# Optimization experiments

Hardware: AMD Instinct MI355X
Metric: run time of the kernel (lower is better)

## Reference

```python
import jax, jax.numpy as jnp
import numpy as np


def _resize_bilinear_ac(x, Ht, Wt):
    # bilinear resize with align_corners=True; x: [B,C,h,w] -> [B,C,Ht,Wt]
    B, C, h, w = x.shape
    ys = jnp.linspace(0.0, h - 1.0, Ht)
    xs = jnp.linspace(0.0, w - 1.0, Wt)
    y0 = jnp.floor(ys).astype(jnp.int32)
    y1 = jnp.minimum(y0 + 1, h - 1)
    x0 = jnp.floor(xs).astype(jnp.int32)
    x1 = jnp.minimum(x0 + 1, w - 1)
    wy = (ys - y0).astype(x.dtype)[None, None, :, None]
    wx = (xs - x0).astype(x.dtype)[None, None, None, :]
    r0 = x[:, :, y0, :]
    r1 = x[:, :, y1, :]
    v00 = r0[:, :, :, x0]; v01 = r0[:, :, :, x1]
    v10 = r1[:, :, :, x0]; v11 = r1[:, :, :, x1]
    return (1 - wy) * ((1 - wx) * v00 + wx * v01) + wy * ((1 - wx) * v10 + wx * v11)


def _grid_sample_zeros_ac(img, grid):
    # F.grid_sample(mode='bilinear', padding_mode='zeros', align_corners=True)
    # img: [B,C,H,W], grid: [B,H,W,2] in [-1,1] (x, y)
    B, C, H, W = img.shape
    x = (grid[..., 0] + 1.0) * 0.5 * (W - 1)  # [B,H,W] pixel coords
    y = (grid[..., 1] + 1.0) * 0.5 * (H - 1)
    x0 = jnp.floor(x)
    y0 = jnp.floor(y)
    wx = (x - x0)[:, None]  # [B,1,H,W]
    wy = (y - y0)[:, None]

    def gather(xi, yi):
        valid = ((xi >= 0) & (xi <= W - 1) & (yi >= 0) & (yi <= H - 1)).astype(img.dtype)
        xc = jnp.clip(xi, 0, W - 1).astype(jnp.int32)
        yc = jnp.clip(yi, 0, H - 1).astype(jnp.int32)
        v = jax.vmap(lambda im, yy, xx: im[:, yy, xx])(img, yc, xc)  # [B,C,H,W]
        return v * valid[:, None]

    v00 = gather(x0, y0)
    v01 = gather(x0 + 1, y0)
    v10 = gather(x0, y0 + 1)
    v11 = gather(x0 + 1, y0 + 1)
    return (1 - wy) * ((1 - wx) * v00 + wx * v01) + wy * ((1 - wx) * v10 + wx * v11)


def setup_inputs() -> dict:
    key = jax.random.key(0)
    k1, k2, k3 = jax.random.split(key, 3)
    B, C, H, W = 8, 3, 384, 1280
    h, w = 96, 320
    image = jax.random.normal(k1, (B, C, H, W), dtype=jnp.float32)
    # positive disparity (fraction of width, scaled by W inside forward)
    disp = jax.random.uniform(k2, (B, 1, h, w), dtype=jnp.float32, minval=0.01, maxval=0.3)
    scene = jax.random.normal(k3, (B, 3, h, w), dtype=jnp.float32) * 0.1
    K = jnp.array([[371.0, 0.0, 320.0], [0.0, 371.0, 96.0], [0.0, 0.0, 1.0]], dtype=jnp.float32)
    intrinsic = jnp.tile(K[None], (B, 1, 1))
    aug_size = jnp.tile(jnp.array([192.0, 640.0], dtype=jnp.float32)[None], (B, 1))
    return {"image": image, "disp": disp, "scene": scene, "intrinsic": intrinsic, "aug_size": aug_size}


def reference(image, disp, scene, intrinsic, aug_size):
    B, C, H, W = image.shape
    # interpolate_as(disp, image) * W
    disp_full = _resize_bilinear_ac(disp, H, W) * W
    # rel_scale = local_scale / aug_size, local_scale = (H, W)
    rel = jnp.array([H, W], dtype=aug_size.dtype) / aug_size  # [B,2] = (sy, sx)
    sy, sx = rel[:, 0], rel[:, 1]
    fx = intrinsic[:, 0, 0] * sx
    fy = intrinsic[:, 1, 1] * sy
    cx = intrinsic[:, 0, 2] * sx
    cy = intrinsic[:, 1, 2] * sy
    z = jnp.zeros_like(fx)
    o = jnp.ones_like(fx)
    K = jnp.stack([jnp.stack([fx, z, cx], 1),
                   jnp.stack([z, fy, cy], 1),
                   jnp.stack([z, z, o], 1)], 1)  # [B,3,3]
    # disp2depth_stereo_clamp
    depth = jnp.clip(fx[:, None, None, None] * 0.54 / (disp_full + 1e-8), 0.001, 80.0)
    # pixel2point
    xg, yg = jnp.meshgrid(jnp.arange(W, dtype=jnp.float32), jnp.arange(H, dtype=jnp.float32))  # [H,W]
    pix = jnp.stack([xg.ravel(), yg.ravel(), jnp.ones(H * W, dtype=jnp.float32)], 0)  # [3,HW]
    Kinv = jnp.linalg.inv(K)
    point = jnp.einsum('bij,jn->bin', Kinv, pix) * depth.reshape(B, 1, -1)  # [B,3,HW]
    # point2pixel_ms
    scene_full = _resize_bilinear_ac(scene, H, W)
    point_form = point.reshape(B, 3, H, W) + scene_full
    proj = jnp.einsum('bij,bjn->bin', K, point_form.reshape(B, 3, -1))
    coord = (proj[:, 0:2] / (proj[:, 2:3] + 1e-8)).reshape(B, 2, H, W)
    nx = coord[:, 0] / (W - 1) * 2.0 - 1.0
    ny = coord[:, 1] / (H - 1) * 2.0 - 1.0
    grid = jnp.stack([nx, ny], -1)  # [B,H,W,2]
    return _grid_sample_zeros_ac(image, grid)
```

## Files before the change

kernel.cpp:

```cpp
#include <hip/hip_runtime.h>
#include <hip/hip_fp16.h>

#define BATCH 8
#define CH 3
#define H_OUT 384
#define W_OUT 1280
#define H_IN 96
#define W_IN 320
#define HW_OUT (H_OUT * W_OUT)
#define HW_IN (H_IN * W_IN)

#define ROWS_PT 2
#define SEGS_PER_ROW (W_OUT / 256)
#define PAIRS (H_OUT / ROWS_PT)
#define CHUNKS_PER_B (PAIRS * SEGS_PER_ROW)

#define LCOLS 68
#define LROWS 3

#define PSTRIDE 1282
#define PK_HALVES ((size_t)(1 + (size_t)BATCH * H_OUT * PSTRIDE) * 4)
#define PK_BYTES (PK_HALVES * 2)

struct __attribute__((packed, aligned(4))) f2 { float x, y; };
struct __attribute__((packed, aligned(8))) h8 { unsigned int w[4]; };

__global__ __launch_bounds__(256) void pack_kernel(
    const float* __restrict__ image, __half* __restrict__ pk)
{
    int i = blockIdx.x * 256 + threadIdx.x;
    int b = i / HW_OUT;
    int p = i - b * HW_OUT;
    int y = p / W_OUT;
    int x = p - y * W_OUT;
    const float* ib = image + (size_t)b * (CH * HW_OUT) + p;
    float c0 = ib[0];
    float c1 = ib[HW_OUT];
    float c2 = ib[2 * HW_OUT];
    __half2 lo = __floats2half2_rn(c0, c1);
    __half2 hi = __floats2half2_rn(c2, 0.0f);
    uint2 v;
    v.x = *reinterpret_cast<unsigned int*>(&lo);
    v.y = *reinterpret_cast<unsigned int*>(&hi);
    __half* pd = pk + 4;
    size_t row = (size_t)b * H_OUT + y;
    *reinterpret_cast<uint2*>(pd + (row * PSTRIDE + x) * 4) = v;

    if (i < BATCH * H_OUT) {
        uint2 z; z.x = 0u; z.y = 0u;
        size_t r = (size_t)i;
        *reinterpret_cast<uint2*>(pd + (r * PSTRIDE + 1280) * 4) = z;
        *reinterpret_cast<uint2*>(pd + (r * PSTRIDE + 1281) * 4) = z;
        if (i == 0) *reinterpret_cast<uint2*>(pk) = z;
    }
}

template <bool PACKED>
__global__ __launch_bounds__(256) void warp_sceneflow_kernel(
    const float* __restrict__ image,
    const __half* __restrict__ pk,
    const float* __restrict__ disp,
    const float* __restrict__ scene,
    const float* __restrict__ intrin,
    const float* __restrict__ aug,
    float* __restrict__ out)
{
    int bid = blockIdx.x;
    int b = bid & 7;
    int c = bid >> 3;
    int yp = c / SEGS_PER_ROW;
    int xseg = c - yp * SEGS_PER_ROW;
    int x = xseg * 256 + threadIdx.x;
    int ybase = yp * ROWS_PT;

    __shared__ float4 lds4[LROWS][LCOLS];
    int ylo = (int)((float)ybase * ((float)(H_IN - 1) / (float)(H_OUT - 1)));
    int xlo = (int)((float)(xseg * 256) * ((float)(W_IN - 1) / (float)(W_OUT - 1)));
    if (threadIdx.x < LROWS * LCOLS) {
        int row = threadIdx.x / LCOLS;
        int col = threadIdx.x - row * LCOLS;
        int gy = min(ylo + row, H_IN - 1);
        int gx = min(xlo + col, W_IN - 1);
        int gi = gy * W_IN + gx;
        const float* dp = disp + b * HW_IN;
        const float* sp = scene + b * (CH * HW_IN);
        float4 v;
        v.x = dp[gi];
        v.y = sp[gi];
        v.z = sp[HW_IN + gi];
        v.w = sp[2 * HW_IN + gi];
        lds4[row][col] = v;
    }
    __syncthreads();

    float sy = (float)H_OUT / aug[b * 2 + 0];
    float sxs = (float)W_OUT / aug[b * 2 + 1];
    float fx = intrin[b * 9 + 0] * sxs;
    float fy = intrin[b * 9 + 4] * sy;
    float cx = intrin[b * 9 + 2] * sxs;
    float cy = intrin[b * 9 + 5] * sy;
    float inv_fx = 1.0f / fx;
    float inv_fy = 1.0f / fy;

    float xsrc = (float)x * ((float)(W_IN - 1) / (float)(W_OUT - 1));
    int x0 = (int)xsrc;
    float wx = xsrc - (float)x0;
    int lx = x0 - xlo;

    float g00[ROWS_PT], g01[ROWS_PT], g10[ROWS_PT], g11[ROWS_PT];
    int rb0[ROWS_PT], rb1[ROWS_PT];
    bool rc[ROWS_PT], lc[ROWS_PT];

    #pragma unroll
    for (int r = 0; r < ROWS_PT; ++r) {
        int y = ybase + r;
        float ysrc = (float)y * ((float)(H_IN - 1) / (float)(H_OUT - 1));
        int y0 = (int)ysrc;
        float wy = ysrc - (float)y0;
        int ly = y0 - ylo;

        float4 t00 = lds4[ly][lx];
        float4 t01 = lds4[ly][lx + 1];
        float4 t10 = lds4[ly + 1][lx];
        float4 t11 = lds4[ly + 1][lx + 1];

        float w00 = (1.0f - wy) * (1.0f - wx);
        float w01 = (1.0f - wy) * wx;
        float w10 = wy * (1.0f - wx);
        float w11 = wy * wx;

        float dval = w00 * t00.x + w01 * t01.x + w10 * t10.x + w11 * t11.x;
        float sc0  = w00 * t00.y + w01 * t01.y + w10 * t10.y + w11 * t11.y;
        float sc1  = w00 * t00.z + w01 * t01.z + w10 * t10.z + w11 * t11.z;
        float sc2  = w00 * t00.w + w01 * t01.w + w10 * t10.w + w11 * t11.w;

        float disp_full = dval * (float)W_OUT;
        float depth = fminf(fmaxf(fx * 0.54f / (disp_full + 1e-8f), 0.001f), 80.0f);

        float X = ((float)x - cx) * inv_fx * depth + sc0;
        float Y = ((float)y - cy) * inv_fy * depth + sc1;
        float Z = depth + sc2;
        float u = fx * X + cx * Z;
        float v = fy * Y + cy * Z;
        float rw = 1.0f / (Z + 1e-8f);
        float gx = u * rw;
        float gy = v * rw;

        float gx0f = floorf(gx), gy0f = floorf(gy);
        float fwx = gx - gx0f, fwy = gy - gy0f;
        int ix0 = (int)gx0f, iy0 = (int)gy0f;
        int ix1 = ix0 + 1, iy1 = iy0 + 1;
        bool vx0 = (ix0 >= 0) && (ix0 <= W_OUT - 1);
        bool vx1 = (ix1 >= 0) && (ix1 <= W_OUT - 1);
        bool vy0 = (iy0 >= 0) && (iy0 <= H_OUT - 1);
        bool vy1 = (iy1 >= 0) && (iy1 <= H_OUT - 1);
        int cy0 = min(max(iy0, 0), H_OUT - 1);
        int cy1 = min(max(iy1, 0), H_OUT - 1);
        g00[r] = (1.0f - fwy) * (1.0f - fwx) * ((vx0 && vy0) ? 1.0f : 0.0f);
        g01[r] = (1.0f - fwy) * fwx * ((vx1 && vy0) ? 1.0f : 0.0f);
        g10[r] = fwy * (1.0f - fwx) * ((vx0 && vy1) ? 1.0f : 0.0f);
        g11[r] = fwy * fwx * ((vx1 && vy1) ? 1.0f : 0.0f);

        if constexpr (PACKED) {
            int bx = min(max(ix0, -1), W_OUT - 1);
            rb0[r] = ((b * H_OUT + cy0) * PSTRIDE + bx);
            rb1[r] = ((b * H_OUT + cy1) * PSTRIDE + bx);
        } else {
            int cx0 = min(max(ix0, 0), W_OUT - 1);
            int cx1 = min(max(ix1, 0), W_OUT - 1);
            int xbi = min(cx0, W_OUT - 2);
            rc[r] = (cx0 != xbi);
            lc[r] = (cx1 == xbi);
            rb0[r] = cy0 * W_OUT + xbi;
            rb1[r] = cy1 * W_OUT + xbi;
        }
    }

    float res[ROWS_PT][CH];
    if constexpr (PACKED) {
        const __half* pd = pk + 4;
        #pragma unroll
        for (int r = 0; r < ROWS_PT; ++r) {
            h8 L0 = *reinterpret_cast<const h8*>(pd + (size_t)rb0[r] * 4);
            h8 L1 = *reinterpret_cast<const h8*>(pd + (size_t)rb1[r] * 4);
            __half2 h0a = *reinterpret_cast<__half2*>(&L0.w[0]);
            __half2 h0b = *reinterpret_cast<__half2*>(&L0.w[1]);
            __half2 h1a = *reinterpret_cast<__half2*>(&L0.w[2]);
            __half2 h1b = *reinterpret_cast<__half2*>(&L0.w[3]);
            __half2 k0a = *reinterpret_cast<__half2*>(&L1.w[0]);
            __half2 k0b = *reinterpret_cast<__half2*>(&L1.w[1]);
            __half2 k1a = *reinterpret_cast<__half2*>(&L1.w[2]);
            __half2 k1b = *reinterpret_cast<__half2*>(&L1.w[3]);
            res[r][0] = g00[r] * __low2float(h0a) + g01[r] * __low2float(h1a)
                      + g10[r] * __low2float(k0a) + g11[r] * __low2float(k1a);
            res[r][1] = g00[r] * __high2float(h0a) + g01[r] * __high2float(h1a)
                      + g10[r] * __high2float(k0a) + g11[r] * __high2float(k1a);
            res[r][2] = g00[r] * __low2float(h0b) + g01[r] * __low2float(h1b)
                      + g10[r] * __low2float(k0b) + g11[r] * __low2float(k1b);
        }
    } else {
        const float* ib = image + (size_t)b * (CH * HW_OUT);
        const float* im0 = ib;
        const float* im1 = ib + HW_OUT;
        const float* im2 = ib + 2 * HW_OUT;
        #pragma unroll
        for (int r = 0; r < ROWS_PT; ++r) {
            f2 P0 = *(const f2*)(im0 + rb0[r]); f2 P1 = *(const f2*)(im0 + rb1[r]);
            f2 Q0 = *(const f2*)(im1 + rb0[r]); f2 Q1 = *(const f2*)(im1 + rb1[r]);
            f2 T0 = *(const f2*)(im2 + rb0[r]); f2 T1 = *(const f2*)(im2 + rb1[r]);
            float p00 = rc[r] ? P0.y : P0.x, p01 = lc[r] ? P0.x : P0.y;
            float p10 = rc[r] ? P1.y : P1.x, p11 = lc[r] ? P1.x : P1.y;
            float q00 = rc[r] ? Q0.y : Q0.x, q01 = lc[r] ? Q0.x : Q0.y;
            float q10 = rc[r] ? Q1.y : Q1.x, q11 = lc[r] ? Q1.x : Q1.y;
            float t00 = rc[r] ? T0.y : T0.x, t01 = lc[r] ? T0.x : T0.y;
            float t10 = rc[r] ? T1.y : T1.x, t11 = lc[r] ? T1.x : T1.y;
            res[r][0] = g00[r] * p00 + g01[r] * p01 + g10[r] * p10 + g11[r] * p11;
            res[r][1] = g00[r] * q00 + g01[r] * q01 + g10[r] * q10 + g11[r] * q11;
            res[r][2] = g00[r] * t00 + g01[r] * t01 + g10[r] * t10 + g11[r] * t11;
        }
    }

    float* ob = out + (size_t)b * (CH * HW_OUT);
    #pragma unroll
    for (int r = 0; r < ROWS_PT; ++r) {
        int op = (ybase + r) * W_OUT + x;
        __builtin_nontemporal_store(res[r][0], ob + op);
        __builtin_nontemporal_store(res[r][1], ob + HW_OUT + op);
        __builtin_nontemporal_store(res[r][2], ob + 2 * HW_OUT + op);
    }
}

extern "C" void kernel_launch(void* const* d_in, const int* in_sizes, int n_in,
                              void* d_out, int out_size, void* d_ws, size_t ws_size,
                              hipStream_t stream) {
    const float* image  = (const float*)d_in[0];
    const float* disp   = (const float*)d_in[1];
    const float* scene  = (const float*)d_in[2];
    const float* intrin = (const float*)d_in[3];
    const float* aug    = (const float*)d_in[4];
    float* out = (float*)d_out;

    const int grid = BATCH * CHUNKS_PER_B;

    if (ws_size >= PK_BYTES) {
        __half* pk = (__half*)d_ws;
        pack_kernel<<<BATCH * HW_OUT / 256, 256, 0, stream>>>(image, pk);
        warp_sceneflow_kernel<true><<<grid, 256, 0, stream>>>(
            image, pk, disp, scene, intrin, aug, out);
    } else {
        warp_sceneflow_kernel<false><<<grid, 256, 0, stream>>>(
            image, nullptr, disp, scene, intrin, aug, out);
    }
}
```

Baseline: 54.66 us.

## Pack vertically adjacent row pairs so each bilinear tap pair is one 16-byte load

Adds a row-pair packed layout in fp16 where each entry holds a pixel's three channels for rows y-1 and y, padded with a zero border. The gather then needs two aligned 16-byte loads per output instead of two loads spread across separate rows. Blending is done with half2 FMAs instead of fp32 math. In exchange the workspace is about twice as large and the pack kernel reads each image row twice, and fp16 accumulation adds precision error.

```diff
diff --git a/kernel.cpp b/kernel.cpp
--- a/kernel.cpp
+++ b/kernel.cpp
@@ -18,14 +18,60 @@
 #define LCOLS 68
 #define LROWS 3
 
-#define PSTRIDE 1282
-#define PK_HALVES ((size_t)(1 + (size_t)BATCH * H_OUT * PSTRIDE) * 4)
-#define PK_BYTES (PK_HALVES * 2)
+#define P1STRIDE 1282
+#define P1_HALVES ((size_t)(1 + (size_t)BATCH * H_OUT * P1STRIDE) * 4)
+#define P1_BYTES (P1_HALVES * 2)
+
+#define RP_STRIDE 1282
+#define RP_ROWS (H_OUT + 1)
+#define RP_EPB ((size_t)RP_ROWS * RP_STRIDE)
+#define RP_ENTRIES ((size_t)BATCH * RP_EPB)
+#define RP_BYTES (RP_ENTRIES * 16)
 
 struct __attribute__((packed, aligned(4))) f2 { float x, y; };
 struct __attribute__((packed, aligned(8))) h8 { unsigned int w[4]; };
-
-__global__ __launch_bounds__(256) void pack_kernel(
+struct __attribute__((aligned(16))) h16 { unsigned int w[4]; };
+
+static __device__ __forceinline__ __half2 u2h2(unsigned int u) {
+    return *reinterpret_cast<__half2*>(&u);
+}
+
+__global__ __launch_bounds__(256) void pack_rowpair_kernel(
+    const float* __restrict__ image, __half* __restrict__ pk)
+{
+    size_t i = (size_t)blockIdx.x * 256 + threadIdx.x;
+    if (i >= RP_ENTRIES) return;
+    int b = (int)(i / RP_EPB);
+    int rem = (int)(i - (size_t)b * RP_EPB);
+    int e = rem / RP_STRIDE;
+    int cxi = rem - e * RP_STRIDE;
+    int x = cxi - 1;
+
+    __half2 p0 = __floats2half2_rn(0.0f, 0.0f);
+    __half2 p1 = p0, p2 = p0, p3 = p0;
+    if (x >= 0 && x < W_OUT) {
+        const float* ib = image + (size_t)b * (CH * HW_OUT);
+        int y0 = e - 1, y1 = e;
+        if (y0 >= 0) {
+            int o = y0 * W_OUT + x;
+            p0 = __floats2half2_rn(ib[o], ib[HW_OUT + o]);
+            p1 = __floats2half2_rn(ib[2 * HW_OUT + o], 0.0f);
+        }
+        if (y1 < H_OUT) {
+            int o = y1 * W_OUT + x;
+            p2 = __floats2half2_rn(ib[o], ib[HW_OUT + o]);
+            p3 = __floats2half2_rn(ib[2 * HW_OUT + o], 0.0f);
+        }
+    }
+    h16 v;
+    v.w[0] = *reinterpret_cast<unsigned int*>(&p0);
+    v.w[1] = *reinterpret_cast<unsigned int*>(&p1);
+    v.w[2] = *reinterpret_cast<unsigned int*>(&p2);
+    v.w[3] = *reinterpret_cast<unsigned int*>(&p3);
+    *reinterpret_cast<h16*>(pk + i * 8) = v;
+}
+
+__global__ __launch_bounds__(256) void pack_single_kernel(
     const float* __restrict__ image, __half* __restrict__ pk)
 {
     int i = blockIdx.x * 256 + threadIdx.x;
@@ -34,28 +80,24 @@
     int y = p / W_OUT;
     int x = p - y * W_OUT;
     const float* ib = image + (size_t)b * (CH * HW_OUT) + p;
-    float c0 = ib[0];
-    float c1 = ib[HW_OUT];
-    float c2 = ib[2 * HW_OUT];
-    __half2 lo = __floats2half2_rn(c0, c1);
-    __half2 hi = __floats2half2_rn(c2, 0.0f);
+    __half2 lo = __floats2half2_rn(ib[0], ib[HW_OUT]);
+    __half2 hi = __floats2half2_rn(ib[2 * HW_OUT], 0.0f);
     uint2 v;
     v.x = *reinterpret_cast<unsigned int*>(&lo);
     v.y = *reinterpret_cast<unsigned int*>(&hi);
     __half* pd = pk + 4;
     size_t row = (size_t)b * H_OUT + y;
-    *reinterpret_cast<uint2*>(pd + (row * PSTRIDE + x) * 4) = v;
-
+    *reinterpret_cast<uint2*>(pd + (row * P1STRIDE + x) * 4) = v;
     if (i < BATCH * H_OUT) {
         uint2 z; z.x = 0u; z.y = 0u;
         size_t r = (size_t)i;
-        *reinterpret_cast<uint2*>(pd + (r * PSTRIDE + 1280) * 4) = z;
-        *reinterpret_cast<uint2*>(pd + (r * PSTRIDE + 1281) * 4) = z;
+        *reinterpret_cast<uint2*>(pd + (r * P1STRIDE + 1280) * 4) = z;
+        *reinterpret_cast<uint2*>(pd + (r * P1STRIDE + 1281) * 4) = z;
         if (i == 0) *reinterpret_cast<uint2*>(pk) = z;
     }
 }
 
-template <bool PACKED>
+template <int MODE>
 __global__ __launch_bounds__(256) void warp_sceneflow_kernel(
     const float* __restrict__ image,
     const __half* __restrict__ pk,
@@ -154,18 +196,25 @@
         bool vx1 = (ix1 >= 0) && (ix1 <= W_OUT - 1);
         bool vy0 = (iy0 >= 0) && (iy0 <= H_OUT - 1);
         bool vy1 = (iy1 >= 0) && (iy1 <= H_OUT - 1);
-        int cy0 = min(max(iy0, 0), H_OUT - 1);
-        int cy1 = min(max(iy1, 0), H_OUT - 1);
         g00[r] = (1.0f - fwy) * (1.0f - fwx) * ((vx0 && vy0) ? 1.0f : 0.0f);
         g01[r] = (1.0f - fwy) * fwx * ((vx1 && vy0) ? 1.0f : 0.0f);
         g10[r] = fwy * (1.0f - fwx) * ((vx0 && vy1) ? 1.0f : 0.0f);
         g11[r] = fwy * fwx * ((vx1 && vy1) ? 1.0f : 0.0f);
 
-        if constexpr (PACKED) {
+        if constexpr (MODE == 2) {
+            int e   = min(max(iy0 + 1, 0), H_OUT);
+            int cxi = min(max(ix0 + 1, 0), W_OUT);
+            rb0[r] = (b * RP_ROWS + e) * RP_STRIDE + cxi;
+            rb1[r] = 0;
+        } else if constexpr (MODE == 1) {
+            int cy0 = min(max(iy0, 0), H_OUT - 1);
+            int cy1 = min(max(iy1, 0), H_OUT - 1);
             int bx = min(max(ix0, -1), W_OUT - 1);
-            rb0[r] = ((b * H_OUT + cy0) * PSTRIDE + bx);
-            rb1[r] = ((b * H_OUT + cy1) * PSTRIDE + bx);
+            rb0[r] = ((b * H_OUT + cy0) * P1STRIDE + bx);
+            rb1[r] = ((b * H_OUT + cy1) * P1STRIDE + bx);
         } else {
+            int cy0 = min(max(iy0, 0), H_OUT - 1);
+            int cy1 = min(max(iy1, 0), H_OUT - 1);
             int cx0 = min(max(ix0, 0), W_OUT - 1);
             int cx1 = min(max(ix1, 0), W_OUT - 1);
             int xbi = min(cx0, W_OUT - 2);
@@ -177,20 +226,38 @@
     }
 
     float res[ROWS_PT][CH];
-    if constexpr (PACKED) {
+    if constexpr (MODE == 2) {
+        #pragma unroll
+        for (int r = 0; r < ROWS_PT; ++r) {
+            h16 L0 = *reinterpret_cast<const h16*>(pk + (size_t)rb0[r] * 8);
+            h16 L1 = *reinterpret_cast<const h16*>(pk + (size_t)rb0[r] * 8 + 8);
+            __half2 G00 = __float2half2_rn(g00[r]);
+            __half2 G01 = __float2half2_rn(g01[r]);
+            __half2 G10 = __float2half2_rn(g10[r]);
+            __half2 G11 = __float2half2_rn(g11[r]);
+            __half2 acc01 = __hmul2(G00, u2h2(L0.w[0]));
+            acc01 = __hfma2(G10, u2h2(L0.w[2]), acc01);
+            acc01 = __hfma2(G01, u2h2(L1.w[0]), acc01);
+            acc01 = __hfma2(G11, u2h2(L1.w[2]), acc01);
+            __half2 acc2 = __hmul2(G00, u2h2(L0.w[1]));
+            acc2 = __hfma2(G10, u2h2(L0.w[3]), acc2);
+            acc2 = __hfma2(G01, u2h2(L1.w[1]), acc2);
+            acc2 = __hfma2(G11, u2h2(L1.w[3]), acc2);
+            float2 f01 = __half22float2(acc01);
+            res[r][0] = f01.x;
+            res[r][1] = f01.y;
+            res[r][2] = __low2float(acc2);
+        }
+    } else if constexpr (MODE == 1) {
         const __half* pd = pk + 4;
         #pragma unroll
         for (int r = 0; r < ROWS_PT; ++r) {
             h8 L0 = *reinterpret_cast<const h8*>(pd + (size_t)rb0[r] * 4);
             h8 L1 = *reinterpret_cast<const h8*>(pd + (size_t)rb1[r] * 4);
-            __half2 h0a = *reinterpret_cast<__half2*>(&L0.w[0]);
-            __half2 h0b = *reinterpret_cast<__half2*>(&L0.w[1]);
-            __half2 h1a = *reinterpret_cast<__half2*>(&L0.w[2]);
-            __half2 h1b = *reinterpret_cast<__half2*>(&L0.w[3]);
-            __half2 k0a = *reinterpret_cast<__half2*>(&L1.w[0]);
-            __half2 k0b = *reinterpret_cast<__half2*>(&L1.w[1]);
-            __half2 k1a = *reinterpret_cast<__half2*>(&L1.w[2]);
-            __half2 k1b = *reinterpret_cast<__half2*>(&L1.w[3]);
+            __half2 h0a = u2h2(L0.w[0]), h0b = u2h2(L0.w[1]);
+            __half2 h1a = u2h2(L0.w[2]), h1b = u2h2(L0.w[3]);
+            __half2 k0a = u2h2(L1.w[0]), k0b = u2h2(L1.w[1]);
+            __half2 k1a = u2h2(L1.w[2]), k1b = u2h2(L1.w[3]);
             res[r][0] = g00[r] * __low2float(h0a) + g01[r] * __low2float(h1a)
                       + g10[r] * __low2float(k0a) + g11[r] * __low2float(k1a);
             res[r][1] = g00[r] * __high2float(h0a) + g01[r] * __high2float(h1a)
@@ -242,13 +309,19 @@
 
     const int grid = BATCH * CHUNKS_PER_B;
 
-    if (ws_size >= PK_BYTES) {
+    if (ws_size >= RP_BYTES) {
         __half* pk = (__half*)d_ws;
-        pack_kernel<<<BATCH * HW_OUT / 256, 256, 0, stream>>>(image, pk);
-        warp_sceneflow_kernel<true><<<grid, 256, 0, stream>>>(
+        const int pgrid = (int)((RP_ENTRIES + 255) / 256);
+        pack_rowpair_kernel<<<pgrid, 256, 0, stream>>>(image, pk);
+        warp_sceneflow_kernel<2><<<grid, 256, 0, stream>>>(
+            image, pk, disp, scene, intrin, aug, out);
+    } else if (ws_size >= P1_BYTES) {
+        __half* pk = (__half*)d_ws;
+        pack_single_kernel<<<BATCH * HW_OUT / 256, 256, 0, stream>>>(image, pk);
+        warp_sceneflow_kernel<1><<<grid, 256, 0, stream>>>(
             image, pk, disp, scene, intrin, aug, out);
     } else {
-        warp_sceneflow_kernel<false><<<grid, 256, 0, stream>>>(
+        warp_sceneflow_kernel<0><<<grid, 256, 0, stream>>>(
             image, nullptr, disp, scene, intrin, aug, out);
     }
 }
```

New measurement: 62.55 us. 14.4% more time.

## Remap warp kernel threads to 2D 16x4 tiles per wave, one pixel each

Applied to the files above, without the earlier changes.

Replaces the 256-wide by 2-row strip per block with a 64x4 pixel block, where each wave covers a 16x4 tile and each thread handles one output pixel. The intent is better gather locality into the packed fp16 image: neighbouring rows in a wave hit nearby cache lines, so the data-dependent bilinear fetches should reuse L1/L2 more. The cost is twice as many blocks, each with less work. Output stores now form 16-wide segments per row instead of full 256-wide rows, which reduces write coalescing.

```diff
diff --git a/kernel.cpp b/kernel.cpp
--- a/kernel.cpp
+++ b/kernel.cpp
@@ -10,22 +10,25 @@
 #define HW_OUT (H_OUT * W_OUT)
 #define HW_IN (H_IN * W_IN)
 
-#define ROWS_PT 2
-#define SEGS_PER_ROW (W_OUT / 256)
-#define PAIRS (H_OUT / ROWS_PT)
-#define CHUNKS_PER_B (PAIRS * SEGS_PER_ROW)
-
-#define LCOLS 68
+#define XS_PER_ROW 20
+#define YSEGS (H_OUT / 4)
+#define CHUNKS_PER_B (YSEGS * XS_PER_ROW)
+
+#define LCOLS 18
 #define LROWS 3
 
-#define PSTRIDE 1282
-#define PK_HALVES ((size_t)(1 + (size_t)BATCH * H_OUT * PSTRIDE) * 4)
-#define PK_BYTES (PK_HALVES * 2)
+#define P1STRIDE 1282
+#define P1_HALVES ((size_t)(1 + (size_t)BATCH * H_OUT * P1STRIDE) * 4)
+#define P1_BYTES (P1_HALVES * 2)
 
 struct __attribute__((packed, aligned(4))) f2 { float x, y; };
 struct __attribute__((packed, aligned(8))) h8 { unsigned int w[4]; };
 
-__global__ __launch_bounds__(256) void pack_kernel(
+static __device__ __forceinline__ __half2 u2h2(unsigned int u) {
+    return *reinterpret_cast<__half2*>(&u);
+}
+
+__global__ __launch_bounds__(256) void pack_single_kernel(
     const float* __restrict__ image, __half* __restrict__ pk)
 {
     int i = blockIdx.x * 256 + threadIdx.x;
@@ -34,28 +37,24 @@
     int y = p / W_OUT;
     int x = p - y * W_OUT;
     const float* ib = image + (size_t)b * (CH * HW_OUT) + p;
-    float c0 = ib[0];
-    float c1 = ib[HW_OUT];
-    float c2 = ib[2 * HW_OUT];
-    __half2 lo = __floats2half2_rn(c0, c1);
-    __half2 hi = __floats2half2_rn(c2, 0.0f);
+    __half2 lo = __floats2half2_rn(ib[0], ib[HW_OUT]);
+    __half2 hi = __floats2half2_rn(ib[2 * HW_OUT], 0.0f);
     uint2 v;
     v.x = *reinterpret_cast<unsigned int*>(&lo);
     v.y = *reinterpret_cast<unsigned int*>(&hi);
     __half* pd = pk + 4;
     size_t row = (size_t)b * H_OUT + y;
-    *reinterpret_cast<uint2*>(pd + (row * PSTRIDE + x) * 4) = v;
-
+    *reinterpret_cast<uint2*>(pd + (row * P1STRIDE + x) * 4) = v;
     if (i < BATCH * H_OUT) {
         uint2 z; z.x = 0u; z.y = 0u;
         size_t r = (size_t)i;
-        *reinterpret_cast<uint2*>(pd + (r * PSTRIDE + 1280) * 4) = z;
-        *reinterpret_cast<uint2*>(pd + (r * PSTRIDE + 1281) * 4) = z;
+        *reinterpret_cast<uint2*>(pd + (r * P1STRIDE + 1280) * 4) = z;
+        *reinterpret_cast<uint2*>(pd + (r * P1STRIDE + 1281) * 4) = z;
         if (i == 0) *reinterpret_cast<uint2*>(pk) = z;
     }
 }
 
-template <bool PACKED>
+template <int MODE>
 __global__ __launch_bounds__(256) void warp_sceneflow_kernel(
     const float* __restrict__ image,
     const __half* __restrict__ pk,
@@ -68,17 +67,25 @@
     int bid = blockIdx.x;
     int b = bid & 7;
     int c = bid >> 3;
-    int yp = c / SEGS_PER_ROW;
-    int xseg = c - yp * SEGS_PER_ROW;
-    int x = xseg * 256 + threadIdx.x;
-    int ybase = yp * ROWS_PT;
+    int ys = c / XS_PER_ROW;
+    int xs = c - ys * XS_PER_ROW;
+    int ybase = ys * 4;
+    int xbase = xs * 64;
+
+    int tid = threadIdx.x;
+    int wave = tid >> 6;
+    int lane = tid & 63;
+    int lx16 = lane & 15;
+    int ly4  = lane >> 4;
+    int x = xbase + wave * 16 + lx16;
+    int y = ybase + ly4;
 
     __shared__ float4 lds4[LROWS][LCOLS];
     int ylo = (int)((float)ybase * ((float)(H_IN - 1) / (float)(H_OUT - 1)));
-    int xlo = (int)((float)(xseg * 256) * ((float)(W_IN - 1) / (float)(W_OUT - 1)));
-    if (threadIdx.x < LROWS * LCOLS) {
-        int row = threadIdx.x / LCOLS;
-        int col = threadIdx.x - row * LCOLS;
+    int xlo = (int)((float)xbase * ((float)(W_IN - 1) / (float)(W_OUT - 1)));
+    if (tid < LROWS * LCOLS) {
+        int row = tid / LCOLS;
+        int col = tid - row * LCOLS;
         int gy = min(ylo + row, H_IN - 1);
         int gx = min(xlo + col, W_IN - 1);
         int gi = gy * W_IN + gx;
@@ -93,12 +100,12 @@
     }
     __syncthreads();
 
-    float sy = (float)H_OUT / aug[b * 2 + 0];
-    float sxs = (float)W_OUT / aug[b * 2 + 1];
-    float fx = intrin[b * 9 + 0] * sxs;
-    float fy = intrin[b * 9 + 4] * sy;
-    float cx = intrin[b * 9 + 2] * sxs;
-    float cy = intrin[b * 9 + 5] * sy;
+    float syr = (float)H_OUT / aug[b * 2 + 0];
+    float sxr = (float)W_OUT / aug[b * 2 + 1];
+    float fx = intrin[b * 9 + 0] * sxr;
+    float fy = intrin[b * 9 + 4] * syr;
+    float cx = intrin[b * 9 + 2] * sxr;
+    float cy = intrin[b * 9 + 5] * syr;
     float inv_fx = 1.0f / fx;
     float inv_fy = 1.0f / fy;
 
@@ -107,127 +114,103 @@
     float wx = xsrc - (float)x0;
     int lx = x0 - xlo;
 
-    float g00[ROWS_PT], g01[ROWS_PT], g10[ROWS_PT], g11[ROWS_PT];
-    int rb0[ROWS_PT], rb1[ROWS_PT];
-    bool rc[ROWS_PT], lc[ROWS_PT];
-
-    #pragma unroll
-    for (int r = 0; r < ROWS_PT; ++r) {
-        int y = ybase + r;
-        float ysrc = (float)y * ((float)(H_IN - 1) / (float)(H_OUT - 1));
-        int y0 = (int)ysrc;
-        float wy = ysrc - (float)y0;
-        int ly = y0 - ylo;
-
-        float4 t00 = lds4[ly][lx];
-        float4 t01 = lds4[ly][lx + 1];
-        float4 t10 = lds4[ly + 1][lx];
-        float4 t11 = lds4[ly + 1][lx + 1];
-
-        float w00 = (1.0f - wy) * (1.0f - wx);
-        float w01 = (1.0f - wy) * wx;
-        float w10 = wy * (1.0f - wx);
-        float w11 = wy * wx;
-
-        float dval = w00 * t00.x + w01 * t01.x + w10 * t10.x + w11 * t11.x;
-        float sc0  = w00 * t00.y + w01 * t01.y + w10 * t10.y + w11 * t11.y;
-        float sc1  = w00 * t00.z + w01 * t01.z + w10 * t10.z + w11 * t11.z;
-        float sc2  = w00 * t00.w + w01 * t01.w + w10 * t10.w + w11 * t11.w;
-
-        float disp_full = dval * (float)W_OUT;
-        float depth = fminf(fmaxf(fx * 0.54f / (disp_full + 1e-8f), 0.001f), 80.0f);
-
-        float X = ((float)x - cx) * inv_fx * depth + sc0;
-        float Y = ((float)y - cy) * inv_fy * depth + sc1;
-        float Z = depth + sc2;
-        float u = fx * X + cx * Z;
-        float v = fy * Y + cy * Z;
-        float rw = 1.0f / (Z + 1e-8f);
-        float gx = u * rw;
-        float gy = v * rw;
-
-        float gx0f = floorf(gx), gy0f = floorf(gy);
-        float fwx = gx - gx0f, fwy = gy - gy0f;
-        int ix0 = (int)gx0f, iy0 = (int)gy0f;
-        int ix1 = ix0 + 1, iy1 = iy0 + 1;
-        bool vx0 = (ix0 >= 0) && (ix0 <= W_OUT - 1);
-        bool vx1 = (ix1 >= 0) && (ix1 <= W_OUT - 1);
-        bool vy0 = (iy0 >= 0) && (iy0 <= H_OUT - 1);
-        bool vy1 = (iy1 >= 0) && (iy1 <= H_OUT - 1);
-        int cy0 = min(max(iy0, 0), H_OUT - 1);
-        int cy1 = min(max(iy1, 0), H_OUT - 1);
-        g00[r] = (1.0f - fwy) * (1.0f - fwx) * ((vx0 && vy0) ? 1.0f : 0.0f);
-        g01[r] = (1.0f - fwy) * fwx * ((vx1 && vy0) ? 1.0f : 0.0f);
-        g10[r] = fwy * (1.0f - fwx) * ((vx0 && vy1) ? 1.0f : 0.0f);
-        g11[r] = fwy * fwx * ((vx1 && vy1) ? 1.0f : 0.0f);
-
-        if constexpr (PACKED) {
-            int bx = min(max(ix0, -1), W_OUT - 1);
-            rb0[r] = ((b * H_OUT + cy0) * PSTRIDE + bx);
-            rb1[r] = ((b * H_OUT + cy1) * PSTRIDE + bx);
-        } else {
-            int cx0 = min(max(ix0, 0), W_OUT - 1);
-            int cx1 = min(max(ix1, 0), W_OUT - 1);
-            int xbi = min(cx0, W_OUT - 2);
-            rc[r] = (cx0 != xbi);
-            lc[r] = (cx1 == xbi);
-            rb0[r] = cy0 * W_OUT + xbi;
-            rb1[r] = cy1 * W_OUT + xbi;
-        }
-    }
-
-    float res[ROWS_PT][CH];
-    if constexpr (PACKED) {
+    float ysrc = (float)y * ((float)(H_IN - 1) / (float)(H_OUT - 1));
+    int y0 = (int)ysrc;
+    float wy = ysrc - (float)y0;
+    int ly = y0 - ylo;
+
+    float4 t00 = lds4[ly][lx];
+    float4 t01 = lds4[ly][lx + 1];
+    float4 t10 = lds4[ly + 1][lx];
+    float4 t11 = lds4[ly + 1][lx + 1];
+
+    float w00 = (1.0f - wy) * (1.0f - wx);
+    float w01 = (1.0f - wy) * wx;
+    float w10 = wy * (1.0f - wx);
+    float w11 = wy * wx;
+
+    float dval = w00 * t00.x + w01 * t01.x + w10 * t10.x + w11 * t11.x;
+    float sc0  = w00 * t00.y + w01 * t01.y + w10 * t10.y + w11 * t11.y;
+    float sc1  = w00 * t00.z + w01 * t01.z + w10 * t10.z + w11 * t11.z;
+    float sc2  = w00 * t00.w + w01 * t01.w + w10 * t10.w + w11 * t11.w;
+
+    float disp_full = dval * (float)W_OUT;
+    float depth = fminf(fmaxf(fx * 0.54f / (disp_full + 1e-8f), 0.001f), 80.0f);
+
+    float X = ((float)x - cx) * inv_fx * depth + sc0;
+    float Y = ((float)y - cy) * inv_fy * depth + sc1;
+    float Z = depth + sc2;
+    float u = fx * X + cx * Z;
+    float v = fy * Y + cy * Z;
+    float rw = 1.0f / (Z + 1e-8f);
+    float gx = u * rw;
+    float gy = v * rw;
+
+    int ix0 = __float2int_rd(gx);
+    int iy0 = __float2int_rd(gy);
+    float fwx = gx - (float)ix0;
+    float fwy = gy - (float)iy0;
+    int ix1 = ix0 + 1, iy1 = iy0 + 1;
+    bool vx0 = (ix0 >= 0) && (ix0 <= W_OUT - 1);
+    bool vx1 = (ix1 >= 0) && (ix1 <= W_OUT - 1);
+    bool vy0 = (iy0 >= 0) && (iy0 <= H_OUT - 1);
+    bool vy1 = (iy1 >= 0) && (iy1 <= H_OUT - 1);
+    float g00 = (1.0f - fwy) * (1.0f - fwx) * ((vx0 && vy0) ? 1.0f : 0.0f);
+    float g01 = (1.0f - fwy) * fwx * ((vx1 && vy0) ? 1.0f : 0.0f);
+    float g10 = fwy * (1.0f - fwx) * ((vx0 && vy1) ? 1.0f : 0.0f);
+    float g11 = fwy * fwx * ((vx1 && vy1) ? 1.0f : 0.0f);
+    int cy0 = min(max(iy0, 0), H_OUT - 1);
+    int cy1 = min(max(iy1, 0), H_OUT - 1);
+
+    float r0, r1, r2;
+    if constexpr (MODE == 1) {
+        int bx = min(max(ix0, -1), W_OUT - 1);
         const __half* pd = pk + 4;
-        #pragma unroll
-        for (int r = 0; r < ROWS_PT; ++r) {
-            h8 L0 = *reinterpret_cast<const h8*>(pd + (size_t)rb0[r] * 4);
-            h8 L1 = *reinterpret_cast<const h8*>(pd + (size_t)rb1[r] * 4);
-            __half2 h0a = *reinterpret_cast<__half2*>(&L0.w[0]);
-            __half2 h0b = *reinterpret_cast<__half2*>(&L0.w[1]);
-            __half2 h1a = *reinterpret_cast<__half2*>(&L0.w[2]);
-            __half2 h1b = *reinterpret_cast<__half2*>(&L0.w[3]);
-            __half2 k0a = *reinterpret_cast<__half2*>(&L1.w[0]);
-            __half2 k0b = *reinterpret_cast<__half2*>(&L1.w[1]);
-            __half2 k1a = *reinterpret_cast<__half2*>(&L1.w[2]);
-            __half2 k1b = *reinterpret_cast<__half2*>(&L1.w[3]);
-            res[r][0] = g00[r] * __low2float(h0a) + g01[r] * __low2float(h1a)
-                      + g10[r] * __low2float(k0a) + g11[r] * __low2float(k1a);
-            res[r][1] = g00[r] * __high2float(h0a) + g01[r] * __high2float(h1a)
-                      + g10[r] * __high2float(k0a) + g11[r] * __high2float(k1a);
-            res[r][2] = g00[r] * __low2float(h0b) + g01[r] * __low2float(h1b)
-                      + g10[r] * __low2float(k0b) + g11[r] * __low2float(k1b);
-        }
+        size_t rb0 = ((size_t)(b * H_OUT + cy0) * P1STRIDE + bx);
+        size_t rb1 = ((size_t)(b * H_OUT + cy1) * P1STRIDE + bx);
+        h8 L0 = *reinterpret_cast<const h8*>(pd + rb0 * 4);
+        h8 L1 = *reinterpret_cast<const h8*>(pd + rb1 * 4);
+        __half2 h0a = u2h2(L0.w[0]), h0b = u2h2(L0.w[1]);
+        __half2 h1a = u2h2(L0.w[2]), h1b = u2h2(L0.w[3]);
+        __half2 k0a = u2h2(L1.w[0]), k0b = u2h2(L1.w[1]);
+        __half2 k1a = u2h2(L1.w[2]), k1b = u2h2(L1.w[3]);
+        r0 = g00 * __low2float(h0a) + g01 * __low2float(h1a)
+           + g10 * __low2float(k0a) + g11 * __low2float(k1a);
+        r1 = g00 * __high2float(h0a) + g01 * __high2float(h1a)
+           + g10 * __high2float(k0a) + g11 * __high2float(k1a);
+        r2 = g00 * __low2float(h0b) + g01 * __low2float(h1b)
+           + g10 * __low2float(k0b) + g11 * __low2float(k1b);
     } else {
+        int cx0 = min(max(ix0, 0), W_OUT - 1);
+        int cx1 = min(max(ix1, 0), W_OUT - 1);
+        int xbi = min(cx0, W_OUT - 2);
+        bool rcf = (cx0 != xbi);
+        bool lcf = (cx1 == xbi);
+        int rb0 = cy0 * W_OUT + xbi;
+        int rb1 = cy1 * W_OUT + xbi;
         const float* ib = image + (size_t)b * (CH * HW_OUT);
         const float* im0 = ib;
         const float* im1 = ib + HW_OUT;
         const float* im2 = ib + 2 * HW_OUT;
-        #pragma unroll
-        for (int r = 0; r < ROWS_PT; ++r) {
-            f2 P0 = *(const f2*)(im0 + rb0[r]); f2 P1 = *(const f2*)(im0 + rb1[r]);
-            f2 Q0 = *(const f2*)(im1 + rb0[r]); f2 Q1 = *(const f2*)(im1 + rb1[r]);
-            f2 T0 = *(const f2*)(im2 + rb0[r]); f2 T1 = *(const f2*)(im2 + rb1[r]);
-            float p00 = rc[r] ? P0.y : P0.x, p01 = lc[r] ? P0.x : P0.y;
-            float p10 = rc[r] ? P1.y : P1.x, p11 = lc[r] ? P1.x : P1.y;
-            float q00 = rc[r] ? Q0.y : Q0.x, q01 = lc[r] ? Q0.x : Q0.y;
-            float q10 = rc[r] ? Q1.y : Q1.x, q11 = lc[r] ? Q1.x : Q1.y;
-            float t00 = rc[r] ? T0.y : T0.x, t01 = lc[r] ? T0.x : T0.y;
-            float t10 = rc[r] ? T1.y : T1.x, t11 = lc[r] ? T1.x : T1.y;
-            res[r][0] = g00[r] * p00 + g01[r] * p01 + g10[r] * p10 + g11[r] * p11;
-            res[r][1] = g00[r] * q00 + g01[r] * q01 + g10[r] * q10 + g11[r] * q11;
-            res[r][2] = g00[r] * t00 + g01[r] * t01 + g10[r] * t10 + g11[r] * t11;
-        }
+        f2 P0 = *(const f2*)(im0 + rb0); f2 P1 = *(const f2*)(im0 + rb1);
+        f2 Q0 = *(const f2*)(im1 + rb0); f2 Q1 = *(const f2*)(im1 + rb1);
+        f2 T0 = *(const f2*)(im2 + rb0); f2 T1 = *(const f2*)(im2 + rb1);
+        float p00 = rcf ? P0.y : P0.x, p01 = lcf ? P0.x : P0.y;
+        float p10 = rcf ? P1.y : P1.x, p11 = lcf ? P1.x : P1.y;
+        float q00 = rcf ? Q0.y : Q0.x, q01 = lcf ? Q0.x : Q0.y;
+        float q10 = rcf ? Q1.y : Q1.x, q11 = lcf ? Q1.x : Q1.y;
+        float t00f = rcf ? T0.y : T0.x, t01f = lcf ? T0.x : T0.y;
+        float t10f = rcf ? T1.y : T1.x, t11f = lcf ? T1.x : T1.y;
+        r0 = g00 * p00 + g01 * p01 + g10 * p10 + g11 * p11;
+        r1 = g00 * q00 + g01 * q01 + g10 * q10 + g11 * q11;
+        r2 = g00 * t00f + g01 * t01f + g10 * t10f + g11 * t11f;
     }
 
     float* ob = out + (size_t)b * (CH * HW_OUT);
-    #pragma unroll
-    for (int r = 0; r < ROWS_PT; ++r) {
-        int op = (ybase + r) * W_OUT + x;
-        __builtin_nontemporal_store(res[r][0], ob + op);
-        __builtin_nontemporal_store(res[r][1], ob + HW_OUT + op);
-        __builtin_nontemporal_store(res[r][2], ob + 2 * HW_OUT + op);
-    }
+    int op = y * W_OUT + x;
+    __builtin_nontemporal_store(r0, ob + op);
+    __builtin_nontemporal_store(r1, ob + HW_OUT + op);
+    __builtin_nontemporal_store(r2, ob + 2 * HW_OUT + op);
 }
 
 extern "C" void kernel_launch(void* const* d_in, const int* in_sizes, int n_in,
@@ -242,13 +225,13 @@
 
     const int grid = BATCH * CHUNKS_PER_B;
 
-    if (ws_size >= PK_BYTES) {
+    if (ws_size >= P1_BYTES) {
         __half* pk = (__half*)d_ws;
-        pack_kernel<<<BATCH * HW_OUT / 256, 256, 0, stream>>>(image, pk);
-        warp_sceneflow_kernel<true><<<grid, 256, 0, stream>>>(
+        pack_single_kernel<<<BATCH * HW_OUT / 256, 256, 0, stream>>>(image, pk);
+        warp_sceneflow_kernel<1><<<grid, 256, 0, stream>>>(
             image, pk, disp, scene, intrin, aug, out);
     } else {
-        warp_sceneflow_kernel<false><<<grid, 256, 0, stream>>>(
+        warp_sceneflow_kernel<0><<<grid, 256, 0, stream>>>(
             image, nullptr, disp, scene, intrin, aug, out);
     }
 }
```

Result: faster. 52.12 us (-4.7%).
